# Kernel optimization log

Hardware: AMD Instinct MI355X
Metric: run time of the kernel (lower is better)

The kernel has to match this reference:

```python
import jax, jax.numpy as jnp
import numpy as np

# Static config matching init_kwargs
LA = 20.0
GAMMA_INV = 1.0 / 0.1   # self.gamma = 1/gamma
TAU = 0.2
MARGIN = 0.01 * 1.0      # margin * margin_scale
CN = 2
K = 2048
DIM = 128
SUMK = CN * K
B = 16384

# Static intra-class upper-triangular pair mask (same as self.weight in torch)
_blk = np.triu(np.ones((K, K), dtype=bool), k=1)
PAIR_MASK = np.zeros((SUMK, SUMK), dtype=bool)
for _i in range(CN):
    PAIR_MASK[_i * K:(_i + 1) * K, _i * K:(_i + 1) * K] = _blk
PAIR_MASK = jnp.asarray(PAIR_MASK)
N_PAIRS = float(CN * K * (K - 1) // 2)


def setup_inputs() -> dict:
    key = jax.random.key(0)
    k1, k2, k3 = jax.random.split(key, 3)
    x = jax.random.normal(k1, (B, DIM), dtype=jnp.float32)
    target = jax.random.randint(k2, (B,), 0, CN, dtype=jnp.int64)
    fc = jax.random.normal(k3, (DIM, SUMK), dtype=jnp.float32) * 0.05
    return {"x": x, "target": target, "fc": fc}


def reference(x, target, fc):
    # L2-normalize inputs (dim=1) and centers (dim=0)
    norm_input = x / jnp.linalg.norm(x, axis=1, keepdims=True)          # [B, DIM]
    centers = fc / jnp.linalg.norm(fc, axis=0, keepdims=True)           # [DIM, SUMK]

    simInd = norm_input @ centers                                       # [B, SUMK]
    sim = simInd.reshape(B, CN, K)                                      # per-class groups

    # softmax-weighted intra-class similarity (intra_max='softmax')
    prob = jax.nn.softmax(sim * GAMMA_INV, axis=-1)
    simClass = jnp.sum(prob * sim, axis=-1)                             # [B, CN]

    # NOTE: original code sets margin on ALL columns, so uniform shift
    logits = LA * (simClass - MARGIN)

    # cross-entropy, mean reduction (class weights are all 1)
    logp = jax.nn.log_softmax(logits, axis=-1)
    ce = -jnp.take_along_axis(logp, target[:, None].astype(jnp.int32), axis=1).mean()

    # center-pair regularizer (tau > 0, K > 1)
    simCenter = centers.T @ centers                                     # [SUMK, SUMK]
    d = jnp.sqrt(2.0 + 1e-5 - 2.0 * simCenter)                          # >=0 everywhere
    reg = jnp.sum(jnp.where(PAIR_MASK, d, 0.0)) / (N_PAIRS * 2.0)

    loss = ce + TAU * reg
    return loss, logits
```

## Files before the change

kernel.cpp:

```cpp
#include <hip/hip_runtime.h>
#include <math.h>

#define NB 16384
#define DIM 128
#define SUMK 4096
#define KCLS 2048

constexpr float LA = 20.0f;
constexpr float GAMMA_INV = 10.0f;
constexpr float TAU = 0.2f;
constexpr float MARGIN = 0.01f;
constexpr float NPAIRS2 = 8384512.0f;
constexpr float G2L = 14.426950408889634f;
#define CS (8 * NB)

typedef _Float16 half8 __attribute__((ext_vector_type(8)));
typedef float f32x4 __attribute__((ext_vector_type(4)));

#define GLOAD_LDS(SRC, DST)                                                          \
    __builtin_amdgcn_global_load_lds(                                                \
        (const __attribute__((address_space(1))) void*)(SRC),                        \
        (__attribute__((address_space(3))) void*)(DST), 16, 0, 0)

__global__ __launch_bounds__(256) void knorm(const float* __restrict__ fc,
                                             _Float16* __restrict__ cnT) {
    const int t = threadIdx.x;
    const int lane = t & 63;
    const int wid = t >> 6;
    const int c = lane & 15;
    const int q = lane >> 4;
    const int j = blockIdx.x * 64 + wid * 16 + c;

    float v[32];
    const float* p = fc + (size_t)(q * 32) * SUMK + j;
    float ss = 0.f;
#pragma unroll
    for (int i = 0; i < 32; ++i) {
        v[i] = p[(size_t)i * SUMK];
        ss = fmaf(v[i], v[i], ss);
    }
    ss += __shfl_xor(ss, 16);
    ss += __shfl_xor(ss, 32);
    float rn = 1.0f / sqrtf(ss);

    _Float16* w = cnT + (size_t)j * DIM + q * 32;
#pragma unroll
    for (int s = 0; s < 4; ++s) {
        half8 h;
#pragma unroll
        for (int k = 0; k < 8; ++k) h[k] = (_Float16)(v[s * 8 + k] * rn);
        *(half8*)(w + s * 8) = h;
    }
}

__global__ __launch_bounds__(256, 4) void kmain(const float* __restrict__ x,
                                                const _Float16* __restrict__ cnT,
                                                float* __restrict__ pw) {
    __shared__ _Float16 smem[3][2][4][64][8];

    const int t = threadIdx.x;
    const int lane = t & 63;
    const int wid = t >> 6;
    const int m = lane & 15;
    const int kg = lane >> 4;
    const int cls = blockIdx.y;
    const int qz = blockIdx.z;
    const int r0 = blockIdx.x * 128 + wid * 32;

    const int q0 = wid * 2, q1 = wid * 2 + 1;
    const int cf0 = q0 >> 2, tt0 = q0 & 3;
    const int cf1 = q1 >> 2, tt1 = q1 & 3;
    const int colbase = cls * KCLS + qz * 512;
    const _Float16* s0 = cnT + (size_t)(colbase + cf0 * 16 + m) * DIM + tt0 * 32 + kg * 8;
    const _Float16* s1 = cnT + (size_t)(colbase + cf1 * 16 + m) * DIM + tt1 * 32 + kg * 8;
    const size_t CSTEP = (size_t)32 * DIM;

#define STAGE(CH, BUF)                                            \
    do {                                                          \
        GLOAD_LDS(s0 + (size_t)(CH) * CSTEP, &smem[BUF][cf0][tt0][0][0]); \
        GLOAD_LDS(s1 + (size_t)(CH) * CSTEP, &smem[BUF][cf1][tt1][0][0]); \
    } while (0)

    STAGE(0, 0);
    STAGE(1, 1);

    half8 b0[4], b1[4];
#define LOADX(ROW, BF)                                                        \
    do {                                                                      \
        const float* xp = x + (size_t)(ROW)*DIM + kg * 8;                     \
        float xr[4][8];                                                       \
        float ss = 0.f;                                                       \
        _Pragma("unroll") for (int tt = 0; tt < 4; ++tt) {                    \
            float4 f0 = *(const float4*)(xp + tt * 32);                       \
            float4 f1 = *(const float4*)(xp + tt * 32 + 4);                   \
            xr[tt][0] = f0.x; xr[tt][1] = f0.y; xr[tt][2] = f0.z;             \
            xr[tt][3] = f0.w; xr[tt][4] = f1.x; xr[tt][5] = f1.y;             \
            xr[tt][6] = f1.z; xr[tt][7] = f1.w;                               \
            _Pragma("unroll") for (int qq = 0; qq < 8; ++qq)                  \
                ss = fmaf(xr[tt][qq], xr[tt][qq], ss);                        \
        }                                                                     \
        ss += __shfl_xor(ss, 16);                                             \
        ss += __shfl_xor(ss, 32);                                             \
        float rn = 1.0f / sqrtf(ss);                                          \
        _Pragma("unroll") for (int tt = 0; tt < 4; ++tt)                      \
            _Pragma("unroll") for (int qq = 0; qq < 8; ++qq)                  \
                BF[tt][qq] = (_Float16)(xr[tt][qq] * rn);                     \
    } while (0)

    LOADX(r0 + m, b0);
    LOADX(r0 + 16 + m, b1);
#undef LOADX

    float rm0 = -1e30f, rz0 = 0.f, rw0 = 0.f;
    float rm1 = -1e30f, rz1 = 0.f, rw1 = 0.f;

#define EPI(C, RM, RZ, RW)                                                    \
    do {                                                                      \
        float mc = fmaxf(fmaxf(C[0], C[1]), fmaxf(C[2], C[3])) * G2L;         \
        float nm = fmaxf(RM, mc);                                             \
        float sc = exp2f(RM - nm);                                            \
        float e0 = exp2f(fmaf(C[0], G2L, -nm));                               \
        float e1 = exp2f(fmaf(C[1], G2L, -nm));                               \
        float e2 = exp2f(fmaf(C[2], G2L, -nm));                               \
        float e3 = exp2f(fmaf(C[3], G2L, -nm));                               \
        RZ = fmaf(RZ, sc, (e0 + e1) + (e2 + e3));                             \
        RW = fmaf(RW, sc, fmaf(e0, C[0], e1 * C[1]) + fmaf(e2, C[2], e3 * C[3])); \
        RM = nm;                                                              \
    } while (0)

    for (int ch = 0; ch < 16; ++ch) {
        __syncthreads();
        if (ch + 2 < 16) STAGE(ch + 2, (ch + 2) % 3);
        const int b = ch % 3;
#pragma unroll
        for (int cf = 0; cf < 2; ++cf) {
            half8 a0 = *(const half8*)&smem[b][cf][0][lane][0];
            half8 a1 = *(const half8*)&smem[b][cf][1][lane][0];
            half8 a2 = *(const half8*)&smem[b][cf][2][lane][0];
            half8 a3 = *(const half8*)&smem[b][cf][3][lane][0];
            f32x4 c0 = {0.f, 0.f, 0.f, 0.f}, c1 = {0.f, 0.f, 0.f, 0.f};
            c0 = __builtin_amdgcn_mfma_f32_16x16x32_f16(a0, b0[0], c0, 0, 0, 0);
            c1 = __builtin_amdgcn_mfma_f32_16x16x32_f16(a0, b1[0], c1, 0, 0, 0);
            c0 = __builtin_amdgcn_mfma_f32_16x16x32_f16(a1, b0[1], c0, 0, 0, 0);
            c1 = __builtin_amdgcn_mfma_f32_16x16x32_f16(a1, b1[1], c1, 0, 0, 0);
            c0 = __builtin_amdgcn_mfma_f32_16x16x32_f16(a2, b0[2], c0, 0, 0, 0);
            c1 = __builtin_amdgcn_mfma_f32_16x16x32_f16(a2, b1[2], c1, 0, 0, 0);
            c0 = __builtin_amdgcn_mfma_f32_16x16x32_f16(a3, b0[3], c0, 0, 0, 0);
            c1 = __builtin_amdgcn_mfma_f32_16x16x32_f16(a3, b1[3], c1, 0, 0, 0);
            EPI(c0, rm0, rz0, rw0);
            EPI(c1, rm1, rz1, rw1);
        }
    }
#undef EPI
#undef STAGE

#pragma unroll
    for (int off = 16; off <= 32; off <<= 1) {
        {
            float om = __shfl_xor(rm0, off), oz = __shfl_xor(rz0, off), ow = __shfl_xor(rw0, off);
            float nm = fmaxf(rm0, om);
            float ea = exp2f(rm0 - nm), eb = exp2f(om - nm);
            rz0 = rz0 * ea + oz * eb; rw0 = rw0 * ea + ow * eb; rm0 = nm;
        }
        {
            float om = __shfl_xor(rm1, off), oz = __shfl_xor(rz1, off), ow = __shfl_xor(rw1, off);
            float nm = fmaxf(rm1, om);
            float ea = exp2f(rm1 - nm), eb = exp2f(om - nm);
            rz1 = rz1 * ea + oz * eb; rw1 = rw1 * ea + ow * eb; rm1 = nm;
        }
    }

    if (lane < 16) {
        const size_t base = (size_t)(cls * 4 + qz) * NB;
        const int rowA = r0 + m, rowB = r0 + 16 + m;
        pw[0 * CS + base + rowA] = rm0;
        pw[0 * CS + base + rowB] = rm1;
        pw[1 * CS + base + rowA] = rz0;
        pw[1 * CS + base + rowB] = rz1;
        pw[2 * CS + base + rowA] = rw0;
        pw[2 * CS + base + rowB] = rw1;
    }
}

__global__ __launch_bounds__(256) void kce(const float* __restrict__ pw,
                                           const int* __restrict__ tgt,
                                           float* __restrict__ out,
                                           float* __restrict__ ce_acc) {
    int i = blockIdx.x * 256 + threadIdx.x;
    float lg[2];
#pragma unroll
    for (int cls = 0; cls < 2; ++cls) {
        float nm = -1e30f, z = 0.f, w = 0.f;
#pragma unroll
        for (int q = 0; q < 4; ++q) {
            const size_t base = (size_t)(cls * 4 + q) * NB + i;
            float mq = pw[0 * CS + base];
            float zq = pw[1 * CS + base];
            float wq = pw[2 * CS + base];
            float n2 = fmaxf(nm, mq);
            float sa = exp2f(nm - n2), sb = exp2f(mq - n2);
            z = z * sa + zq * sb;
            w = w * sa + wq * sb;
            nm = n2;
        }
        lg[cls] = LA * (w / z - MARGIN);
        out[1 + 2 * i + cls] = lg[cls];
    }
    int tg = tgt[i];
    float mx = fmaxf(lg[0], lg[1]);
    float lse = mx + logf(expf(lg[0] - mx) + expf(lg[1] - mx));
    float ce = lse - (tg ? lg[1] : lg[0]);
#pragma unroll
    for (int off = 1; off < 64; off <<= 1) ce += __shfl_xor(ce, off);
    if ((threadIdx.x & 63) == 0) atomicAdd(ce_acc, ce);
}

__global__ __launch_bounds__(256) void kreg(const _Float16* __restrict__ cnT,
                                            float* __restrict__ reg_acc) {
    const int bid = blockIdx.x;
    const int cls = bid >> 10;
    const int ti = (bid >> 5) & 31;
    const int tj = bid & 31;
    if (tj < ti) return;

    __shared__ float red[4];
    const int t = threadIdx.x;
    const int lane = t & 63;
    const int wid = t >> 6;
    const int m = lane & 15;
    const int kg = lane >> 4;
    const int i0 = cls * KCLS + ti * 64 + wid * 16;
    const int jb = cls * KCLS + tj * 64;

    const _Float16* aip = cnT + (size_t)(i0 + m) * DIM + kg * 8;
    half8 af[4];
#pragma unroll
    for (int tt = 0; tt < 4; ++tt) af[tt] = *(const half8*)(aip + tt * 32);

    half8 bf[16];
#pragma unroll
    for (int fj = 0; fj < 4; ++fj) {
        const _Float16* bjp = cnT + (size_t)(jb + fj * 16 + m) * DIM + kg * 8;
#pragma unroll
        for (int tt = 0; tt < 4; ++tt) bf[fj * 4 + tt] = *(const half8*)(bjp + tt * 32);
    }

    float local = 0.f;
#pragma unroll
    for (int fj = 0; fj < 4; ++fj) {
        f32x4 cc = {0.f, 0.f, 0.f, 0.f};
#pragma unroll
        for (int tt = 0; tt < 4; ++tt)
            cc = __builtin_amdgcn_mfma_f32_16x16x32_f16(af[tt], bf[fj * 4 + tt], cc, 0, 0, 0);
        int gj = jb + fj * 16 + m;
#pragma unroll
        for (int r = 0; r < 4; ++r) {
            int gi = i0 + kg * 4 + r;
            if (gi < gj)
                local += sqrtf(fmaxf(2.0f + 1e-5f - 2.f * cc[r], 0.f));
        }
    }
#pragma unroll
    for (int off = 1; off < 64; off <<= 1) local += __shfl_xor(local, off);
    if (lane == 0) red[wid] = local;
    __syncthreads();
    if (t == 0) atomicAdd(reg_acc, (red[0] + red[1]) + (red[2] + red[3]));
}

__global__ void kfin(const float* __restrict__ accum, float* __restrict__ out) {
    out[0] = accum[0] / (float)NB + TAU * (accum[1] / NPAIRS2);
}

extern "C" void kernel_launch(void* const* d_in, const int* in_sizes, int n_in,
                              void* d_out, int out_size, void* d_ws, size_t ws_size,
                              hipStream_t stream) {
    const float* x  = (const float*)d_in[0];
    const int*   tg = (const int*)d_in[1];
    const float* fc = (const float*)d_in[2];
    float* out = (float*)d_out;
    float* ws  = (float*)d_ws;
    float* accum = ws;
    _Float16* cnT = (_Float16*)(ws + 16);
    float* pw = (float*)(cnT + (size_t)SUMK * DIM);

    hipMemsetAsync(accum, 0, 64, stream);
    knorm<<<SUMK / 64, 256, 0, stream>>>(fc, cnT);
    kmain<<<dim3(NB / 128, 2, 4), 256, 0, stream>>>(x, cnT, pw);
    kreg<<<2048, 256, 0, stream>>>(cnT, accum + 1);
    kce<<<NB / 256, 256, 0, stream>>>(pw, tg, out, accum);
    kfin<<<1, 1, 0, stream>>>(accum, out);
}
```

Measured before the change: 133.4 us.

## Drop online-max softmax tracking and fuse regularizer blocks into main kernel

Result: faster. 117.6 us (-11.8%).

```diff
diff --git a/kernel.cpp b/kernel.cpp
--- a/kernel.cpp
+++ b/kernel.cpp
@@ -7,7 +7,6 @@
 #define KCLS 2048
 
 constexpr float LA = 20.0f;
-constexpr float GAMMA_INV = 10.0f;
 constexpr float TAU = 0.2f;
 constexpr float MARGIN = 0.01f;
 constexpr float NPAIRS2 = 8384512.0f;
@@ -16,6 +15,12 @@
 
 typedef _Float16 half8 __attribute__((ext_vector_type(8)));
 typedef float f32x4 __attribute__((ext_vector_type(4)));
+
+#if __has_builtin(__builtin_amdgcn_exp2f)
+#define EXP2(v) __builtin_amdgcn_exp2f(v)
+#else
+#define EXP2(v) exp2f(v)
+#endif
 
 #define GLOAD_LDS(SRC, DST)                                                          \
     __builtin_amdgcn_global_load_lds(                                                \
@@ -53,19 +58,69 @@
     }
 }
 
-__global__ __launch_bounds__(256, 4) void kmain(const float* __restrict__ x,
-                                                const _Float16* __restrict__ cnT,
-                                                float* __restrict__ pw) {
+__global__ __launch_bounds__(256, 4) void kbig(const float* __restrict__ x,
+                                               const _Float16* __restrict__ cnT,
+                                               float* __restrict__ pw,
+                                               float* __restrict__ reg_acc) {
     __shared__ _Float16 smem[3][2][4][64][8];
+    __shared__ float red[4];
 
     const int t = threadIdx.x;
     const int lane = t & 63;
     const int wid = t >> 6;
     const int m = lane & 15;
     const int kg = lane >> 4;
-    const int cls = blockIdx.y;
-    const int qz = blockIdx.z;
-    const int r0 = blockIdx.x * 128 + wid * 32;
+    const int id = blockIdx.x;
+
+    if (id >= 1024) {
+        const int rid = id - 1024;
+        const int cls = rid >> 10;
+        const int ti = (rid >> 5) & 31;
+        const int tj = rid & 31;
+        if (tj < ti) return;
+
+        const int i0 = cls * KCLS + ti * 64 + wid * 16;
+        const int jb = cls * KCLS + tj * 64;
+
+        const _Float16* aip = cnT + (size_t)(i0 + m) * DIM + kg * 8;
+        half8 af[4];
+#pragma unroll
+        for (int tt = 0; tt < 4; ++tt) af[tt] = *(const half8*)(aip + tt * 32);
+
+        half8 bf[16];
+#pragma unroll
+        for (int fj = 0; fj < 4; ++fj) {
+            const _Float16* bjp = cnT + (size_t)(jb + fj * 16 + m) * DIM + kg * 8;
+#pragma unroll
+            for (int tt = 0; tt < 4; ++tt) bf[fj * 4 + tt] = *(const half8*)(bjp + tt * 32);
+        }
+
+        float local = 0.f;
+#pragma unroll
+        for (int fj = 0; fj < 4; ++fj) {
+            f32x4 cc = {0.f, 0.f, 0.f, 0.f};
+#pragma unroll
+            for (int tt = 0; tt < 4; ++tt)
+                cc = __builtin_amdgcn_mfma_f32_16x16x32_f16(af[tt], bf[fj * 4 + tt], cc, 0, 0, 0);
+            int gj = jb + fj * 16 + m;
+#pragma unroll
+            for (int r = 0; r < 4; ++r) {
+                int gi = i0 + kg * 4 + r;
+                if (gi < gj)
+                    local += sqrtf(fmaxf(2.0f + 1e-5f - 2.f * cc[r], 0.f));
+            }
+        }
+#pragma unroll
+        for (int off = 1; off < 64; off <<= 1) local += __shfl_xor(local, off);
+        if (lane == 0) red[wid] = local;
+        __syncthreads();
+        if (t == 0) atomicAdd(reg_acc, (red[0] + red[1]) + (red[2] + red[3]));
+        return;
+    }
+
+    const int cls = (id >> 7) & 1;
+    const int qz = id >> 8;
+    const int r0 = (id & 127) * 128 + wid * 32;
 
     const int q0 = wid * 2, q1 = wid * 2 + 1;
     const int cf0 = q0 >> 2, tt0 = q0 & 3;
@@ -75,8 +130,8 @@
     const _Float16* s1 = cnT + (size_t)(colbase + cf1 * 16 + m) * DIM + tt1 * 32 + kg * 8;
     const size_t CSTEP = (size_t)32 * DIM;
 
-#define STAGE(CH, BUF)                                            \
-    do {                                                          \
+#define STAGE(CH, BUF)                                                    \
+    do {                                                                  \
         GLOAD_LDS(s0 + (size_t)(CH) * CSTEP, &smem[BUF][cf0][tt0][0][0]); \
         GLOAD_LDS(s1 + (size_t)(CH) * CSTEP, &smem[BUF][cf1][tt1][0][0]); \
     } while (0)
@@ -101,7 +156,7 @@
         }                                                                     \
         ss += __shfl_xor(ss, 16);                                             \
         ss += __shfl_xor(ss, 32);                                             \
-        float rn = 1.0f / sqrtf(ss);                                          \
+        float rn = G2L / sqrtf(ss);                                           \
         _Pragma("unroll") for (int tt = 0; tt < 4; ++tt)                      \
             _Pragma("unroll") for (int qq = 0; qq < 8; ++qq)                  \
                 BF[tt][qq] = (_Float16)(xr[tt][qq] * rn);                     \
@@ -111,21 +166,16 @@
     LOADX(r0 + 16 + m, b1);
 #undef LOADX
 
-    float rm0 = -1e30f, rz0 = 0.f, rw0 = 0.f;
-    float rm1 = -1e30f, rz1 = 0.f, rw1 = 0.f;
-
-#define EPI(C, RM, RZ, RW)                                                    \
+    float rz0 = 0.f, rw0 = 0.f, rz1 = 0.f, rw1 = 0.f;
+
+#define EPI(C, RZ, RW)                                                        \
     do {                                                                      \
-        float mc = fmaxf(fmaxf(C[0], C[1]), fmaxf(C[2], C[3])) * G2L;         \
-        float nm = fmaxf(RM, mc);                                             \
-        float sc = exp2f(RM - nm);                                            \
-        float e0 = exp2f(fmaf(C[0], G2L, -nm));                               \
-        float e1 = exp2f(fmaf(C[1], G2L, -nm));                               \
-        float e2 = exp2f(fmaf(C[2], G2L, -nm));                               \
-        float e3 = exp2f(fmaf(C[3], G2L, -nm));                               \
-        RZ = fmaf(RZ, sc, (e0 + e1) + (e2 + e3));                             \
-        RW = fmaf(RW, sc, fmaf(e0, C[0], e1 * C[1]) + fmaf(e2, C[2], e3 * C[3])); \
-        RM = nm;                                                              \
+        float e0 = EXP2(C[0]);                                                \
+        float e1 = EXP2(C[1]);                                                \
+        float e2 = EXP2(C[2]);                                                \
+        float e3 = EXP2(C[3]);                                                \
+        RZ += (e0 + e1) + (e2 + e3);                                          \
+        RW += fmaf(e0, C[0], e1 * C[1]) + fmaf(e2, C[2], e3 * C[3]);          \
     } while (0)
 
     for (int ch = 0; ch < 16; ++ch) {
@@ -147,38 +197,25 @@
             c1 = __builtin_amdgcn_mfma_f32_16x16x32_f16(a2, b1[2], c1, 0, 0, 0);
             c0 = __builtin_amdgcn_mfma_f32_16x16x32_f16(a3, b0[3], c0, 0, 0, 0);
             c1 = __builtin_amdgcn_mfma_f32_16x16x32_f16(a3, b1[3], c1, 0, 0, 0);
-            EPI(c0, rm0, rz0, rw0);
-            EPI(c1, rm1, rz1, rw1);
+            EPI(c0, rz0, rw0);
+            EPI(c1, rz1, rw1);
         }
     }
 #undef EPI
 #undef STAGE
 
-#pragma unroll
-    for (int off = 16; off <= 32; off <<= 1) {
-        {
-            float om = __shfl_xor(rm0, off), oz = __shfl_xor(rz0, off), ow = __shfl_xor(rw0, off);
-            float nm = fmaxf(rm0, om);
-            float ea = exp2f(rm0 - nm), eb = exp2f(om - nm);
-            rz0 = rz0 * ea + oz * eb; rw0 = rw0 * ea + ow * eb; rm0 = nm;
-        }
-        {
-            float om = __shfl_xor(rm1, off), oz = __shfl_xor(rz1, off), ow = __shfl_xor(rw1, off);
-            float nm = fmaxf(rm1, om);
-            float ea = exp2f(rm1 - nm), eb = exp2f(om - nm);
-            rz1 = rz1 * ea + oz * eb; rw1 = rw1 * ea + ow * eb; rm1 = nm;
-        }
-    }
+    rz0 += __shfl_xor(rz0, 16); rz0 += __shfl_xor(rz0, 32);
+    rw0 += __shfl_xor(rw0, 16); rw0 += __shfl_xor(rw0, 32);
+    rz1 += __shfl_xor(rz1, 16); rz1 += __shfl_xor(rz1, 32);
+    rw1 += __shfl_xor(rw1, 16); rw1 += __shfl_xor(rw1, 32);
 
     if (lane < 16) {
         const size_t base = (size_t)(cls * 4 + qz) * NB;
         const int rowA = r0 + m, rowB = r0 + 16 + m;
-        pw[0 * CS + base + rowA] = rm0;
-        pw[0 * CS + base + rowB] = rm1;
-        pw[1 * CS + base + rowA] = rz0;
-        pw[1 * CS + base + rowB] = rz1;
-        pw[2 * CS + base + rowA] = rw0;
-        pw[2 * CS + base + rowB] = rw1;
+        pw[0 * CS + base + rowA] = rz0;
+        pw[0 * CS + base + rowB] = rz1;
+        pw[1 * CS + base + rowA] = rw0;
+        pw[1 * CS + base + rowB] = rw1;
     }
 }
 
@@ -190,20 +227,14 @@
     float lg[2];
 #pragma unroll
     for (int cls = 0; cls < 2; ++cls) {
-        float nm = -1e30f, z = 0.f, w = 0.f;
+        float z = 0.f, w = 0.f;
 #pragma unroll
         for (int q = 0; q < 4; ++q) {
             const size_t base = (size_t)(cls * 4 + q) * NB + i;
-            float mq = pw[0 * CS + base];
-            float zq = pw[1 * CS + base];
-            float wq = pw[2 * CS + base];
-            float n2 = fmaxf(nm, mq);
-            float sa = exp2f(nm - n2), sb = exp2f(mq - n2);
-            z = z * sa + zq * sb;
-            w = w * sa + wq * sb;
-            nm = n2;
-        }
-        lg[cls] = LA * (w / z - MARGIN);
+            z += pw[0 * CS + base];
+            w += pw[1 * CS + base];
+        }
+        lg[cls] = LA * (w / (z * G2L) - MARGIN);
         out[1 + 2 * i + cls] = lg[cls];
     }
     int tg = tgt[i];
@@ -213,58 +244,6 @@
 #pragma unroll
     for (int off = 1; off < 64; off <<= 1) ce += __shfl_xor(ce, off);
     if ((threadIdx.x & 63) == 0) atomicAdd(ce_acc, ce);
-}
-
-__global__ __launch_bounds__(256) void kreg(const _Float16* __restrict__ cnT,
-                                            float* __restrict__ reg_acc) {
-    const int bid = blockIdx.x;
-    const int cls = bid >> 10;
-    const int ti = (bid >> 5) & 31;
-    const int tj = bid & 31;
-    if (tj < ti) return;
-
-    __shared__ float red[4];
-    const int t = threadIdx.x;
-    const int lane = t & 63;
-    const int wid = t >> 6;
-    const int m = lane & 15;
-    const int kg = lane >> 4;
-    const int i0 = cls * KCLS + ti * 64 + wid * 16;
-    const int jb = cls * KCLS + tj * 64;
-
-    const _Float16* aip = cnT + (size_t)(i0 + m) * DIM + kg * 8;
-    half8 af[4];
-#pragma unroll
-    for (int tt = 0; tt < 4; ++tt) af[tt] = *(const half8*)(aip + tt * 32);
-
-    half8 bf[16];
-#pragma unroll
-    for (int fj = 0; fj < 4; ++fj) {
-        const _Float16* bjp = cnT + (size_t)(jb + fj * 16 + m) * DIM + kg * 8;
-#pragma unroll
-        for (int tt = 0; tt < 4; ++tt) bf[fj * 4 + tt] = *(const half8*)(bjp + tt * 32);
-    }
-
-    float local = 0.f;
-#pragma unroll
-    for (int fj = 0; fj < 4; ++fj) {
-        f32x4 cc = {0.f, 0.f, 0.f, 0.f};
-#pragma unroll
-        for (int tt = 0; tt < 4; ++tt)
-            cc = __builtin_amdgcn_mfma_f32_16x16x32_f16(af[tt], bf[fj * 4 + tt], cc, 0, 0, 0);
-        int gj = jb + fj * 16 + m;
-#pragma unroll
-        for (int r = 0; r < 4; ++r) {
-            int gi = i0 + kg * 4 + r;
-            if (gi < gj)
-                local += sqrtf(fmaxf(2.0f + 1e-5f - 2.f * cc[r], 0.f));
-        }
-    }
-#pragma unroll
-    for (int off = 1; off < 64; off <<= 1) local += __shfl_xor(local, off);
-    if (lane == 0) red[wid] = local;
-    __syncthreads();
-    if (t == 0) atomicAdd(reg_acc, (red[0] + red[1]) + (red[2] + red[3]));
 }
 
 __global__ void kfin(const float* __restrict__ accum, float* __restrict__ out) {
@@ -285,8 +264,7 @@
 
     hipMemsetAsync(accum, 0, 64, stream);
     knorm<<<SUMK / 64, 256, 0, stream>>>(fc, cnT);
-    kmain<<<dim3(NB / 128, 2, 4), 256, 0, stream>>>(x, cnT, pw);
-    kreg<<<2048, 256, 0, stream>>>(cnT, accum + 1);
+    kbig<<<1024 + 2048, 256, 0, stream>>>(x, cnT, pw, accum + 1);
     kce<<<NB / 256, 256, 0, stream>>>(pw, tg, out, accum);
     kfin<<<1, 1, 0, stream>>>(accum, out);
 }
```
